# Performance work log

Measured on AMD Instinct MI355X. Metric: run time of the kernel, lower is better.

Reference implementation:

```python
import jax, jax.numpy as jnp
import numpy as np

N = 50000      # nodes
E = 800000     # edges
D = 96         # nfeat
C = 40         # nclass
NITE = 8       # train_nite / eval_nite
SMOOTH = 0.5   # smooth_fac


def setup_inputs() -> dict:
    key = jax.random.key(0)
    ks = jax.random.split(key, 6)
    x = jax.random.normal(ks[0], (N, D), dtype=jnp.float32)
    edge_row = jax.random.randint(ks[1], (E,), 0, N)
    edge_col = jax.random.randint(ks[2], (E,), 0, N)
    # ~1/avg_degree scale mimics a symmetrically normalized adjacency
    edge_vals = jax.random.uniform(ks[3], (E,), dtype=jnp.float32) / 16.0
    W_gc = jax.random.normal(ks[4], (D, D), dtype=jnp.float32) / jnp.sqrt(jnp.float32(D))
    b_gc = jnp.zeros((D,), dtype=jnp.float32)
    W_lin = jax.random.normal(ks[5], (D, C), dtype=jnp.float32) / jnp.sqrt(jnp.float32(D))
    return {"x": x, "edge_row": edge_row, "edge_col": edge_col,
            "edge_vals": edge_vals, "W_gc": W_gc, "b_gc": b_gc, "W_lin": W_lin}


def reference(x, edge_row, edge_col, edge_vals, W_gc, b_gc, W_lin):
    # One iteration: GraphConvolution (support = h @ W; out = A @ support + b),
    # smoothing skip connection, ReLU. Dropout is identity (eval / rate 0).
    def one_iter(h, _):
        support = h @ W_gc                                   # [N, D]
        msg = support[edge_col] * edge_vals[:, None]         # [E, D] gather + scale
        agg = jax.ops.segment_sum(msg, edge_row, num_segments=N) + b_gc  # [N, D]
        h_new = jax.nn.relu(SMOOTH * h + (1.0 - SMOOTH) * agg)
        return h_new, None

    h, _ = jax.lax.scan(one_iter, x, None, length=NITE)
    logits = h @ W_lin                                       # [N, C]
    return jax.nn.log_softmax(logits, axis=1)
```

## Files before the change

kernel.cpp:

```cpp
#include <hip/hip_runtime.h>

#define N_NODES 50000
#define E_EDGES 800000
#define D_FEAT  96
#define C_CLS   40
#define N_ITER  8

#define NCHUNK 49
#define NB     256
#define EPB    3125

typedef short bf16x8 __attribute__((ext_vector_type(8)));
typedef float f32x4  __attribute__((ext_vector_type(4)));
typedef float f32x2  __attribute__((ext_vector_type(2)));

#if defined(__has_builtin)
#if __has_builtin(__builtin_amdgcn_cvt_pk_f32_fp8) && __has_builtin(__builtin_amdgcn_cvt_pk_fp8_f32)
#define HAVE_FP8_CVT 1
#endif
#endif
#ifndef HAVE_FP8_CVT
#define HAVE_FP8_CVT 0
#endif

static __device__ __forceinline__ unsigned short f2bf(float f) {
    unsigned u = __float_as_uint(f);
    u = (u + 0x7FFF + ((u >> 16) & 1)) >> 16;
    return (unsigned short)u;
}

static __device__ __forceinline__ unsigned f32_to_fp8_manual(float f) {
    unsigned u = __float_as_uint(f);
    unsigned s = u >> 31;
    int e8 = (int)((u >> 23) & 0xFF) - 127 + 7;
    unsigned m23 = u & 0x7FFFFF;
    if (e8 <= 0) return s << 7;
    if (e8 >= 15) return (s << 7) | 0x7E;
    unsigned m = m23 >> 20;
    unsigned rem = m23 & 0xFFFFF;
    if (rem > 0x80000u || (rem == 0x80000u && (m & 1))) {
        m++;
        if (m == 8) { m = 0; e8++; if (e8 >= 15) return (s << 7) | 0x7E; }
    }
    return (s << 7) | ((unsigned)e8 << 3) | m;
}
static __device__ __forceinline__ float fp8_to_f32_manual(unsigned b) {
    unsigned s = (b >> 7) & 1, e = (b >> 3) & 0xF, m = b & 7;
    if (e == 0) return 0.0f;
    return __uint_as_float((s << 31) | ((e + 120) << 23) | (m << 20));
}
static __device__ __forceinline__ void fp8x4_dec(unsigned w, float* o) {
#if HAVE_FP8_CVT
    f32x2 lo = __builtin_amdgcn_cvt_pk_f32_fp8(w, false);
    f32x2 hi = __builtin_amdgcn_cvt_pk_f32_fp8(w, true);
    o[0] = lo[0]; o[1] = lo[1]; o[2] = hi[0]; o[3] = hi[1];
#else
    o[0] = fp8_to_f32_manual(w & 0xFF);
    o[1] = fp8_to_f32_manual((w >> 8) & 0xFF);
    o[2] = fp8_to_f32_manual((w >> 16) & 0xFF);
    o[3] = fp8_to_f32_manual((w >> 24) & 0xFF);
#endif
}
static __device__ __forceinline__ unsigned fp8x4_enc(float a, float b, float c, float d) {
#if HAVE_FP8_CVT
    unsigned w = __builtin_amdgcn_cvt_pk_fp8_f32(a, b, 0, false);
    w = __builtin_amdgcn_cvt_pk_fp8_f32(c, d, (int)w, true);
    return w;
#else
    return f32_to_fp8_manual(a) | (f32_to_fp8_manual(b) << 8) |
           (f32_to_fp8_manual(c) << 16) | (f32_to_fp8_manual(d) << 24);
#endif
}

__global__ __launch_bounds__(256) void k_count(const int* __restrict__ erow,
                                               int* __restrict__ cm) {
    __shared__ int lcnt[NCHUNK];
    int b = blockIdx.x, tid = threadIdx.x;
    if (tid < NCHUNK) lcnt[tid] = 0;
    __syncthreads();
    int base = b * EPB;
    for (int i = tid; i < EPB; i += 256)
        atomicAdd(&lcnt[erow[base + i] >> 10], 1);
    __syncthreads();
    if (tid < NCHUNK) cm[tid * NB + b] = lcnt[tid];
}

__global__ __launch_bounds__(1024) void k_cscan(int* __restrict__ cm) {
    __shared__ int sb[1024];
    const int TOT = NCHUNK * NB;
    const int PER = 13;
    int tid = threadIdx.x;
    int base = tid * PER;
    int v[PER];
    int s = 0;
    #pragma unroll
    for (int j = 0; j < PER; ++j) {
        int idx = base + j;
        v[j] = (idx < TOT) ? cm[idx] : 0;
        s += v[j];
    }
    sb[tid] = s;
    __syncthreads();
    for (int d = 1; d < 1024; d <<= 1) {
        int t = (tid >= d) ? sb[tid - d] : 0;
        __syncthreads();
        sb[tid] += t;
        __syncthreads();
    }
    int ex = sb[tid] - s;
    #pragma unroll
    for (int j = 0; j < PER; ++j) {
        int idx = base + j;
        if (idx < TOT) { cm[idx] = ex; ex += v[j]; }
    }
}

__global__ __launch_bounds__(256) void k_scatter_runs(const int* __restrict__ erow,
                                                      const int* __restrict__ ecol,
                                                      const float* __restrict__ ev,
                                                      const int* __restrict__ cm,
                                                      int2* __restrict__ stag) {
    __shared__ int lcur[NCHUNK];
    int b = blockIdx.x, tid = threadIdx.x;
    if (tid < NCHUNK) lcur[tid] = cm[tid * NB + b];
    __syncthreads();
    int base = b * EPB;
    for (int i = tid; i < EPB; i += 256) {
        int e = base + i;
        int r = erow[e];
        int c = r >> 10;
        int pos = atomicAdd(&lcur[c], 1);
        int2 s;
        s.x = (int)((unsigned)(ecol[e] & 0xFFFF) | ((unsigned)f2bf(ev[e]) << 16));
        s.y = r & 1023;
        stag[pos] = s;
    }
}

__global__ __launch_bounds__(1024) void k_chunk_csr(const int2* __restrict__ stag,
                                                    const int* __restrict__ cm,
                                                    unsigned* __restrict__ epk,
                                                    int* __restrict__ off) {
    __shared__ int lh[1024];
    __shared__ int lex[1024];
    __shared__ int sb[1024];
    int c = blockIdx.x, tid = threadIdx.x;
    int cb = cm[c * NB];
    int ce = (c + 1 < NCHUNK) ? cm[(c + 1) * NB] : E_EDGES;
    int m = ce - cb;

    lh[tid] = 0;
    __syncthreads();
    for (int i = tid; i < m; i += 1024) {
        int2 s = stag[cb + i];
        atomicAdd(&lh[s.y], 1);
    }
    __syncthreads();
    int v = lh[tid];
    sb[tid] = v;
    __syncthreads();
    for (int d = 1; d < 1024; d <<= 1) {
        int t = (tid >= d) ? sb[tid - d] : 0;
        __syncthreads();
        sb[tid] += t;
        __syncthreads();
    }
    int ex = sb[tid] - v;
    lex[tid] = ex;
    int node = c * 1024 + tid;
    if (node < N_NODES) off[node] = cb + ex;
    if (c == NCHUNK - 1 && tid == 0) off[N_NODES] = E_EDGES;
    __syncthreads();
    for (int i = tid; i < m; i += 1024) {
        int2 s = stag[cb + i];
        int pos = atomicAdd(&lex[s.y], 1);
        epk[cb + pos] = (unsigned)s.x;
    }
}

__global__ __launch_bounds__(256) void k_prep_w(const float* __restrict__ W,
                                                unsigned short* __restrict__ WB) {
    for (int idx = threadIdx.x; idx < 18 * 64; idx += 256) {
        int grp = idx >> 6;
        int lane = idx & 63;
        int t = grp / 3, s = grp - t * 3;
        int n = t * 16 + (lane & 15);
        int k0 = s * 32 + (lane >> 4) * 8;
        unsigned short* dst = WB + (size_t)idx * 8;
        #pragma unroll
        for (int j = 0; j < 8; ++j)
            dst[j] = f2bf(W[(k0 + j) * D_FEAT + n]);
    }
}

__global__ __launch_bounds__(256) void k_cvt_bf16(const float* __restrict__ src,
                                                  unsigned short* __restrict__ dst,
                                                  int n8) {
    int g = blockIdx.x * 256 + threadIdx.x;
    if (g >= n8) return;
    const float4* s4 = (const float4*)src + (size_t)g * 2;
    float4 x0 = s4[0], x1 = s4[1];
    float vals[8] = {x0.x, x0.y, x0.z, x0.w, x1.x, x1.y, x1.z, x1.w};
    uint4 pk; unsigned* pku = (unsigned*)&pk;
    #pragma unroll
    for (int w2 = 0; w2 < 4; ++w2) {
        unsigned lo = f2bf(vals[w2 * 2 + 0]);
        unsigned hi = f2bf(vals[w2 * 2 + 1]);
        pku[w2] = lo | (hi << 16);
    }
    *(uint4*)(dst + (size_t)g * 8) = pk;
}

__global__ __launch_bounds__(256) void k_matmul_mfma(
        const unsigned short* __restrict__ hb,
        const unsigned short* __restrict__ WB,
        unsigned char* __restrict__ support) {
    __shared__ float sm[64 * 100];
    int tid = threadIdx.x;
    int wave = tid >> 6, lane = tid & 63;
    int q = lane >> 4, c = lane & 15;
    int m0 = blockIdx.x * 64 + wave * 16;

    if (m0 < N_NODES) {
        const unsigned short* arow = hb + (size_t)(m0 + c) * D_FEAT + q * 8;
        bf16x8 a0 = *(const bf16x8*)(arow);
        bf16x8 a1 = *(const bf16x8*)(arow + 32);
        bf16x8 a2 = *(const bf16x8*)(arow + 64);
        #pragma unroll
        for (int t = 0; t < 6; ++t) {
            const unsigned short* bp = WB + ((size_t)(t * 3) * 64 + lane) * 8;
            bf16x8 b0 = *(const bf16x8*)(bp);
            bf16x8 b1 = *(const bf16x8*)(bp + 64 * 8);
            bf16x8 b2 = *(const bf16x8*)(bp + 128 * 8);
            f32x4 acc = {0.f, 0.f, 0.f, 0.f};
            acc = __builtin_amdgcn_mfma_f32_16x16x32_bf16(a0, b0, acc, 0, 0, 0);
            acc = __builtin_amdgcn_mfma_f32_16x16x32_bf16(a1, b1, acc, 0, 0, 0);
            acc = __builtin_amdgcn_mfma_f32_16x16x32_bf16(a2, b2, acc, 0, 0, 0);
            #pragma unroll
            for (int r = 0; r < 4; ++r)
                sm[(wave * 16 + q * 4 + r) * 100 + t * 16 + c] = acc[r];
        }
    }
    __syncthreads();

    #pragma unroll
    for (int oo = 0; oo < 3; ++oo) {
        int o = tid + oo * 256;
        int row = o / 12;
        int cb = (o - row * 12) * 8;
        int grow = blockIdx.x * 64 + row;
        if (grow < N_NODES) {
            const float* sp = sm + row * 100 + cb;
            uint2 pk;
            pk.x = fp8x4_enc(sp[0], sp[1], sp[2], sp[3]);
            pk.y = fp8x4_enc(sp[4], sp[5], sp[6], sp[7]);
            *(uint2*)(support + (size_t)grow * D_FEAT + cb) = pk;
        }
    }
}

__global__ __launch_bounds__(192) void k_agg(const int* __restrict__ off,
                                             const unsigned* __restrict__ epk,
                                             const unsigned char* __restrict__ support,
                                             const unsigned short* hin,
                                             const float* __restrict__ b,
                                             unsigned short* hout) {
    int gid = blockIdx.x * 192 + threadIdx.x;
    int n = gid / 6;
    int q = gid % 6;
    if (n >= N_NODES) return;

    int s = off[n];
    int e = off[n + 1];

    float acc[16];
    #pragma unroll
    for (int j = 0; j < 16; ++j) acc[j] = 0.0f;

    int i = s;
    for (; i < e && (i & 3); ++i) {
        unsigned p = epk[i];
        float v = __uint_as_float(p & 0xFFFF0000u);
        uint4 r = *(const uint4*)(support + (size_t)(p & 0xFFFFu) * D_FEAT + q * 16);
        float f[16];
        fp8x4_dec(r.x, f); fp8x4_dec(r.y, f + 4);
        fp8x4_dec(r.z, f + 8); fp8x4_dec(r.w, f + 12);
        #pragma unroll
        for (int j = 0; j < 16; ++j) acc[j] = fmaf(f[j], v, acc[j]);
    }
    for (; i + 4 <= e; i += 4) {
        uint4 pq = *(const uint4*)(epk + i);
        const unsigned* pp = (const unsigned*)&pq;
        uint4 r0 = *(const uint4*)(support + (size_t)(pp[0] & 0xFFFFu) * D_FEAT + q * 16);
        uint4 r1 = *(const uint4*)(support + (size_t)(pp[1] & 0xFFFFu) * D_FEAT + q * 16);
        uint4 r2 = *(const uint4*)(support + (size_t)(pp[2] & 0xFFFFu) * D_FEAT + q * 16);
        uint4 r3 = *(const uint4*)(support + (size_t)(pp[3] & 0xFFFFu) * D_FEAT + q * 16);
        float v0 = __uint_as_float(pp[0] & 0xFFFF0000u);
        float v1 = __uint_as_float(pp[1] & 0xFFFF0000u);
        float v2 = __uint_as_float(pp[2] & 0xFFFF0000u);
        float v3 = __uint_as_float(pp[3] & 0xFFFF0000u);
        float f[16];
        fp8x4_dec(r0.x, f); fp8x4_dec(r0.y, f + 4);
        fp8x4_dec(r0.z, f + 8); fp8x4_dec(r0.w, f + 12);
        #pragma unroll
        for (int j = 0; j < 16; ++j) acc[j] = fmaf(f[j], v0, acc[j]);
        fp8x4_dec(r1.x, f); fp8x4_dec(r1.y, f + 4);
        fp8x4_dec(r1.z, f + 8); fp8x4_dec(r1.w, f + 12);
        #pragma unroll
        for (int j = 0; j < 16; ++j) acc[j] = fmaf(f[j], v1, acc[j]);
        fp8x4_dec(r2.x, f); fp8x4_dec(r2.y, f + 4);
        fp8x4_dec(r2.z, f + 8); fp8x4_dec(r2.w, f + 12);
        #pragma unroll
        for (int j = 0; j < 16; ++j) acc[j] = fmaf(f[j], v2, acc[j]);
        fp8x4_dec(r3.x, f); fp8x4_dec(r3.y, f + 4);
        fp8x4_dec(r3.z, f + 8); fp8x4_dec(r3.w, f + 12);
        #pragma unroll
        for (int j = 0; j < 16; ++j) acc[j] = fmaf(f[j], v3, acc[j]);
    }
    for (; i < e; ++i) {
        unsigned p = epk[i];
        float v = __uint_as_float(p & 0xFFFF0000u);
        uint4 r = *(const uint4*)(support + (size_t)(p & 0xFFFFu) * D_FEAT + q * 16);
        float f[16];
        fp8x4_dec(r.x, f); fp8x4_dec(r.y, f + 4);
        fp8x4_dec(r.z, f + 8); fp8x4_dec(r.w, f + 12);
        #pragma unroll
        for (int j = 0; j < 16; ++j) acc[j] = fmaf(f[j], v, acc[j]);
    }

    const unsigned short* hrow = hin + (size_t)n * D_FEAT + q * 16;
    uint4 hq0 = *(const uint4*)(hrow);
    uint4 hq1 = *(const uint4*)(hrow + 8);
    const unsigned* hu0 = (const unsigned*)&hq0;
    const unsigned* hu1 = (const unsigned*)&hq1;
    const float* brow = b + q * 16;
    float og[16];
    #pragma unroll
    for (int w2 = 0; w2 < 4; ++w2) {
        float h0 = __uint_as_float(hu0[w2] << 16);
        float h1 = __uint_as_float(hu0[w2] & 0xFFFF0000u);
        og[w2*2+0] = fmaxf(0.5f * h0 + 0.5f * (acc[w2*2+0] + brow[w2*2+0]), 0.0f);
        og[w2*2+1] = fmaxf(0.5f * h1 + 0.5f * (acc[w2*2+1] + brow[w2*2+1]), 0.0f);
        float h2 = __uint_as_float(hu1[w2] << 16);
        float h3 = __uint_as_float(hu1[w2] & 0xFFFF0000u);
        og[8+w2*2+0] = fmaxf(0.5f * h2 + 0.5f * (acc[8+w2*2+0] + brow[8+w2*2+0]), 0.0f);
        og[8+w2*2+1] = fmaxf(0.5f * h3 + 0.5f * (acc[8+w2*2+1] + brow[8+w2*2+1]), 0.0f);
    }
    uint4 pk0, pk1;
    unsigned* pu0 = (unsigned*)&pk0;
    unsigned* pu1 = (unsigned*)&pk1;
    #pragma unroll
    for (int w2 = 0; w2 < 4; ++w2) {
        pu0[w2] = (unsigned)f2bf(og[w2*2+0]) | ((unsigned)f2bf(og[w2*2+1]) << 16);
        pu1[w2] = (unsigned)f2bf(og[8+w2*2+0]) | ((unsigned)f2bf(og[8+w2*2+1]) << 16);
    }
    unsigned short* orow = hout + (size_t)n * D_FEAT + q * 16;
    *(uint4*)(orow) = pk0;
    *(uint4*)(orow + 8) = pk1;
}

__global__ __launch_bounds__(256) void k_final(const unsigned short* __restrict__ hb,
                                               const float* __restrict__ Wg,
                                               float* __restrict__ out) {
    __shared__ float Wl[D_FEAT * C_CLS];
    {
        const float4* src = (const float4*)Wg;
        float4* dst = (float4*)Wl;
        for (int i = threadIdx.x; i < 960; i += 256) dst[i] = src[i];
    }
    __syncthreads();

    int n = blockIdx.x * 256 + threadIdx.x;
    if (n >= N_NODES) return;

    float acc[C_CLS];
    #pragma unroll
    for (int c = 0; c < C_CLS; ++c) acc[c] = 0.0f;

    const unsigned short* hrow = hb + (size_t)n * D_FEAT;
    for (int g = 0; g < 12; ++g) {
        uint4 hq = *(const uint4*)(hrow + g * 8);
        const unsigned* hu = (const unsigned*)&hq;
        float hv[8];
        #pragma unroll
        for (int w2 = 0; w2 < 4; ++w2) {
            hv[w2*2+0] = __uint_as_float(hu[w2] << 16);
            hv[w2*2+1] = __uint_as_float(hu[w2] & 0xFFFF0000u);
        }
        #pragma unroll
        for (int kk = 0; kk < 8; ++kk) {
            float hs = hv[kk];
            const float* wr = &Wl[(g * 8 + kk) * C_CLS];
            #pragma unroll
            for (int c4 = 0; c4 < 10; ++c4) {
                float4 w = *(const float4*)(wr + c4 * 4);
                acc[c4 * 4 + 0] = fmaf(hs, w.x, acc[c4 * 4 + 0]);
                acc[c4 * 4 + 1] = fmaf(hs, w.y, acc[c4 * 4 + 1]);
                acc[c4 * 4 + 2] = fmaf(hs, w.z, acc[c4 * 4 + 2]);
                acc[c4 * 4 + 3] = fmaf(hs, w.w, acc[c4 * 4 + 3]);
            }
        }
    }

    float m = acc[0];
    #pragma unroll
    for (int c = 1; c < C_CLS; ++c) m = fmaxf(m, acc[c]);
    float s = 0.0f;
    #pragma unroll
    for (int c = 0; c < C_CLS; ++c) s += expf(acc[c] - m);
    float lse = m + logf(s);

    float* orow = out + (size_t)n * C_CLS;
    #pragma unroll
    for (int c4 = 0; c4 < 10; ++c4)
        *(float4*)(orow + c4 * 4) =
            make_float4(acc[c4 * 4 + 0] - lse, acc[c4 * 4 + 1] - lse,
                        acc[c4 * 4 + 2] - lse, acc[c4 * 4 + 3] - lse);
}

static inline size_t align256(size_t x) { return (x + 255) & ~(size_t)255; }

extern "C" void kernel_launch(void* const* d_in, const int* in_sizes, int n_in,
                              void* d_out, int out_size, void* d_ws, size_t ws_size,
                              hipStream_t stream) {
    const float* x    = (const float*)d_in[0];
    const int*   erow = (const int*)  d_in[1];
    const int*   ecol = (const int*)  d_in[2];
    const float* ev   = (const float*)d_in[3];
    const float* Wgc  = (const float*)d_in[4];
    const float* bgc  = (const float*)d_in[5];
    const float* Wlin = (const float*)d_in[6];
    float* out = (float*)d_out;

    const size_t NF = (size_t)N_NODES * D_FEAT;
    char* ws = (char*)d_ws;
    unsigned short* hb         = (unsigned short*)ws; ws += align256(NF * 2);
    unsigned short* xb         = (unsigned short*)ws; ws += align256(NF * 2);
    unsigned char*  support_f8 = (unsigned char*)ws;  ws += align256(NF);
    unsigned*       epk        = (unsigned*)ws;       ws += align256((size_t)E_EDGES * 4);
    int2*           stag       = (int2*)ws;           ws += align256((size_t)E_EDGES * 8);
    unsigned short* WB         = (unsigned short*)ws; ws += align256((size_t)18 * 64 * 8 * 2);
    int*            off        = (int*)ws;            ws += align256((size_t)(N_NODES + 1) * 4);
    int*            cm         = (int*)ws;            ws += align256((size_t)NCHUNK * NB * 4);

    k_prep_w      <<<1, 256, 0, stream>>>(Wgc, WB);
    k_cvt_bf16    <<<(int)((NF / 8 + 255) / 256), 256, 0, stream>>>(x, xb, (int)(NF / 8));
    k_count       <<<NB, 256, 0, stream>>>(erow, cm);
    k_cscan       <<<1, 1024, 0, stream>>>(cm);
    k_scatter_runs<<<NB, 256, 0, stream>>>(erow, ecol, ev, cm, stag);
    k_chunk_csr   <<<NCHUNK, 1024, 0, stream>>>(stag, cm, epk, off);

    const int g_mm = (N_NODES + 63) / 64;
    const int g_ag = (N_NODES * 6 + 191) / 192;
    for (int it = 0; it < N_ITER; ++it) {
        const unsigned short* hin = (it == 0) ? xb : hb;
        k_matmul_mfma<<<g_mm, 256, 0, stream>>>(hin, WB, support_f8);
        k_agg        <<<g_ag, 192, 0, stream>>>(off, epk, support_f8, hin, bgc, hb);
    }
    k_final<<<(N_NODES + 255) / 256, 256, 0, stream>>>(hb, Wlin, out);
}
```

Before: 374.8 us.

## Split fp8 support into two column planes and aggregate each half separately

The matmul now writes the fp8 support matrix as two planes, each holding 48 feature columns per node in a 64-byte row. Aggregation runs as two kernel launches, one per plane, and each thread accumulates 8 features instead of 16. The smaller per-pass gather working set is meant to fit better in the per-XCD L2 cache, and the gather loop is software-pipelined to prefetch the next group of four neighbour rows. In exchange, the CSR edge list is read twice per iteration, there is an extra launch, and the padded rows add some memory footprint.

```diff
diff --git a/kernel.cpp b/kernel.cpp
--- a/kernel.cpp
+++ b/kernel.cpp
@@ -9,6 +9,8 @@
 #define NCHUNK 49
 #define NB     256
 #define EPB    3125
+
+#define PLANE  ((size_t)N_NODES * 64)
 
 typedef short bf16x8 __attribute__((ext_vector_type(8)));
 typedef float f32x4  __attribute__((ext_vector_type(4)));
@@ -72,6 +74,14 @@
 #endif
 }
 
+static __device__ __forceinline__ void fma8(uint2 r, float v, float* acc) {
+    float f[8];
+    fp8x4_dec(r.x, f);
+    fp8x4_dec(r.y, f + 4);
+    #pragma unroll
+    for (int j = 0; j < 8; ++j) acc[j] = fmaf(f[j], v, acc[j]);
+}
+
 __global__ __launch_bounds__(256) void k_count(const int* __restrict__ erow,
                                                int* __restrict__ cm) {
     __shared__ int lcnt[NCHUNK];
@@ -214,7 +224,7 @@
 __global__ __launch_bounds__(256) void k_matmul_mfma(
         const unsigned short* __restrict__ hb,
         const unsigned short* __restrict__ WB,
-        unsigned char* __restrict__ support) {
+        unsigned char* __restrict__ supp) {
     __shared__ float sm[64 * 100];
     int tid = threadIdx.x;
     int wave = tid >> 6, lane = tid & 63;
@@ -243,28 +253,31 @@
     }
     __syncthreads();
 
-    #pragma unroll
-    for (int oo = 0; oo < 3; ++oo) {
-        int o = tid + oo * 256;
-        int row = o / 12;
-        int cb = (o - row * 12) * 8;
+    for (int o = tid; o < 384; o += 256) {
+        int row = o / 6;
+        int rem = o - row * 6;
+        int plane = rem / 3;
+        int q3 = rem - plane * 3;
         int grow = blockIdx.x * 64 + row;
         if (grow < N_NODES) {
-            const float* sp = sm + row * 100 + cb;
-            uint2 pk;
-            pk.x = fp8x4_enc(sp[0], sp[1], sp[2], sp[3]);
-            pk.y = fp8x4_enc(sp[4], sp[5], sp[6], sp[7]);
-            *(uint2*)(support + (size_t)grow * D_FEAT + cb) = pk;
+            const float* sp = sm + row * 100 + plane * 48 + q3 * 16;
+            uint4 pk;
+            pk.x = fp8x4_enc(sp[0],  sp[1],  sp[2],  sp[3]);
+            pk.y = fp8x4_enc(sp[4],  sp[5],  sp[6],  sp[7]);
+            pk.z = fp8x4_enc(sp[8],  sp[9],  sp[10], sp[11]);
+            pk.w = fp8x4_enc(sp[12], sp[13], sp[14], sp[15]);
+            *(uint4*)(supp + (size_t)plane * PLANE + (size_t)grow * 64 + q3 * 16) = pk;
         }
     }
 }
 
-__global__ __launch_bounds__(192) void k_agg(const int* __restrict__ off,
-                                             const unsigned* __restrict__ epk,
-                                             const unsigned char* __restrict__ support,
-                                             const unsigned short* hin,
-                                             const float* __restrict__ b,
-                                             unsigned short* hout) {
+__global__ __launch_bounds__(192) void k_agg_half(const int* __restrict__ off,
+                                                  const unsigned* __restrict__ epk,
+                                                  const unsigned char* __restrict__ plane,
+                                                  const unsigned short* hin,
+                                                  const float* __restrict__ b,
+                                                  unsigned short* hout,
+                                                  int pc) {
     int gid = blockIdx.x * 192 + threadIdx.x;
     int n = gid / 6;
     int q = gid % 6;
@@ -273,90 +286,72 @@
     int s = off[n];
     int e = off[n + 1];
 
-    float acc[16];
-    #pragma unroll
-    for (int j = 0; j < 16; ++j) acc[j] = 0.0f;
+    float acc[8];
+    #pragma unroll
+    for (int j = 0; j < 8; ++j) acc[j] = 0.0f;
+
+    const int qb = q * 8;
 
     int i = s;
     for (; i < e && (i & 3); ++i) {
         unsigned p = epk[i];
         float v = __uint_as_float(p & 0xFFFF0000u);
-        uint4 r = *(const uint4*)(support + (size_t)(p & 0xFFFFu) * D_FEAT + q * 16);
-        float f[16];
-        fp8x4_dec(r.x, f); fp8x4_dec(r.y, f + 4);
-        fp8x4_dec(r.z, f + 8); fp8x4_dec(r.w, f + 12);
-        #pragma unroll
-        for (int j = 0; j < 16; ++j) acc[j] = fmaf(f[j], v, acc[j]);
-    }
-    for (; i + 4 <= e; i += 4) {
+        uint2 r = *(const uint2*)(plane + (size_t)(p & 0xFFFFu) * 64 + qb);
+        fma8(r, v, acc);
+    }
+    int ng = (e - i) >> 2;
+    if (ng > 0) {
         uint4 pq = *(const uint4*)(epk + i);
-        const unsigned* pp = (const unsigned*)&pq;
-        uint4 r0 = *(const uint4*)(support + (size_t)(pp[0] & 0xFFFFu) * D_FEAT + q * 16);
-        uint4 r1 = *(const uint4*)(support + (size_t)(pp[1] & 0xFFFFu) * D_FEAT + q * 16);
-        uint4 r2 = *(const uint4*)(support + (size_t)(pp[2] & 0xFFFFu) * D_FEAT + q * 16);
-        uint4 r3 = *(const uint4*)(support + (size_t)(pp[3] & 0xFFFFu) * D_FEAT + q * 16);
-        float v0 = __uint_as_float(pp[0] & 0xFFFF0000u);
-        float v1 = __uint_as_float(pp[1] & 0xFFFF0000u);
-        float v2 = __uint_as_float(pp[2] & 0xFFFF0000u);
-        float v3 = __uint_as_float(pp[3] & 0xFFFF0000u);
-        float f[16];
-        fp8x4_dec(r0.x, f); fp8x4_dec(r0.y, f + 4);
-        fp8x4_dec(r0.z, f + 8); fp8x4_dec(r0.w, f + 12);
-        #pragma unroll
-        for (int j = 0; j < 16; ++j) acc[j] = fmaf(f[j], v0, acc[j]);
-        fp8x4_dec(r1.x, f); fp8x4_dec(r1.y, f + 4);
-        fp8x4_dec(r1.z, f + 8); fp8x4_dec(r1.w, f + 12);
-        #pragma unroll
-        for (int j = 0; j < 16; ++j) acc[j] = fmaf(f[j], v1, acc[j]);
-        fp8x4_dec(r2.x, f); fp8x4_dec(r2.y, f + 4);
-        fp8x4_dec(r2.z, f + 8); fp8x4_dec(r2.w, f + 12);
-        #pragma unroll
-        for (int j = 0; j < 16; ++j) acc[j] = fmaf(f[j], v2, acc[j]);
-        fp8x4_dec(r3.x, f); fp8x4_dec(r3.y, f + 4);
-        fp8x4_dec(r3.z, f + 8); fp8x4_dec(r3.w, f + 12);
-        #pragma unroll
-        for (int j = 0; j < 16; ++j) acc[j] = fmaf(f[j], v3, acc[j]);
+        uint2 c0 = *(const uint2*)(plane + (size_t)(pq.x & 0xFFFFu) * 64 + qb);
+        uint2 c1 = *(const uint2*)(plane + (size_t)(pq.y & 0xFFFFu) * 64 + qb);
+        uint2 c2 = *(const uint2*)(plane + (size_t)(pq.z & 0xFFFFu) * 64 + qb);
+        uint2 c3 = *(const uint2*)(plane + (size_t)(pq.w & 0xFFFFu) * 64 + qb);
+        float v0 = __uint_as_float(pq.x & 0xFFFF0000u);
+        float v1 = __uint_as_float(pq.y & 0xFFFF0000u);
+        float v2 = __uint_as_float(pq.z & 0xFFFF0000u);
+        float v3 = __uint_as_float(pq.w & 0xFFFF0000u);
+        for (int g = 1; g < ng; ++g) {
+            uint4 pq2 = *(const uint4*)(epk + i + 4 * g);
+            uint2 n0 = *(const uint2*)(plane + (size_t)(pq2.x & 0xFFFFu) * 64 + qb);
+            uint2 n1 = *(const uint2*)(plane + (size_t)(pq2.y & 0xFFFFu) * 64 + qb);
+            uint2 n2 = *(const uint2*)(plane + (size_t)(pq2.z & 0xFFFFu) * 64 + qb);
+            uint2 n3 = *(const uint2*)(plane + (size_t)(pq2.w & 0xFFFFu) * 64 + qb);
+            fma8(c0, v0, acc); fma8(c1, v1, acc);
+            fma8(c2, v2, acc); fma8(c3, v3, acc);
+            c0 = n0; c1 = n1; c2 = n2; c3 = n3;
+            v0 = __uint_as_float(pq2.x & 0xFFFF0000u);
+            v1 = __uint_as_float(pq2.y & 0xFFFF0000u);
+            v2 = __uint_as_float(pq2.z & 0xFFFF0000u);
+            v3 = __uint_as_float(pq2.w & 0xFFFF0000u);
+        }
+        fma8(c0, v0, acc); fma8(c1, v1, acc);
+        fma8(c2, v2, acc); fma8(c3, v3, acc);
+        i += 4 * ng;
     }
     for (; i < e; ++i) {
         unsigned p = epk[i];
         float v = __uint_as_float(p & 0xFFFF0000u);
-        uint4 r = *(const uint4*)(support + (size_t)(p & 0xFFFFu) * D_FEAT + q * 16);
-        float f[16];
-        fp8x4_dec(r.x, f); fp8x4_dec(r.y, f + 4);
-        fp8x4_dec(r.z, f + 8); fp8x4_dec(r.w, f + 12);
-        #pragma unroll
-        for (int j = 0; j < 16; ++j) acc[j] = fmaf(f[j], v, acc[j]);
-    }
-
-    const unsigned short* hrow = hin + (size_t)n * D_FEAT + q * 16;
-    uint4 hq0 = *(const uint4*)(hrow);
-    uint4 hq1 = *(const uint4*)(hrow + 8);
-    const unsigned* hu0 = (const unsigned*)&hq0;
-    const unsigned* hu1 = (const unsigned*)&hq1;
-    const float* brow = b + q * 16;
-    float og[16];
+        uint2 r = *(const uint2*)(plane + (size_t)(p & 0xFFFFu) * 64 + qb);
+        fma8(r, v, acc);
+    }
+
+    int col = pc + qb;
+    uint4 hq = *(const uint4*)(hin + (size_t)n * D_FEAT + col);
+    const unsigned* hu = (const unsigned*)&hq;
+    const float* brow = b + col;
+    float og[8];
     #pragma unroll
     for (int w2 = 0; w2 < 4; ++w2) {
-        float h0 = __uint_as_float(hu0[w2] << 16);
-        float h1 = __uint_as_float(hu0[w2] & 0xFFFF0000u);
+        float h0 = __uint_as_float(hu[w2] << 16);
+        float h1 = __uint_as_float(hu[w2] & 0xFFFF0000u);
         og[w2*2+0] = fmaxf(0.5f * h0 + 0.5f * (acc[w2*2+0] + brow[w2*2+0]), 0.0f);
         og[w2*2+1] = fmaxf(0.5f * h1 + 0.5f * (acc[w2*2+1] + brow[w2*2+1]), 0.0f);
-        float h2 = __uint_as_float(hu1[w2] << 16);
-        float h3 = __uint_as_float(hu1[w2] & 0xFFFF0000u);
-        og[8+w2*2+0] = fmaxf(0.5f * h2 + 0.5f * (acc[8+w2*2+0] + brow[8+w2*2+0]), 0.0f);
-        og[8+w2*2+1] = fmaxf(0.5f * h3 + 0.5f * (acc[8+w2*2+1] + brow[8+w2*2+1]), 0.0f);
-    }
-    uint4 pk0, pk1;
-    unsigned* pu0 = (unsigned*)&pk0;
-    unsigned* pu1 = (unsigned*)&pk1;
-    #pragma unroll
-    for (int w2 = 0; w2 < 4; ++w2) {
-        pu0[w2] = (unsigned)f2bf(og[w2*2+0]) | ((unsigned)f2bf(og[w2*2+1]) << 16);
-        pu1[w2] = (unsigned)f2bf(og[8+w2*2+0]) | ((unsigned)f2bf(og[8+w2*2+1]) << 16);
-    }
-    unsigned short* orow = hout + (size_t)n * D_FEAT + q * 16;
-    *(uint4*)(orow) = pk0;
-    *(uint4*)(orow + 8) = pk1;
+    }
+    uint4 pk; unsigned* pku = (unsigned*)&pk;
+    #pragma unroll
+    for (int w2 = 0; w2 < 4; ++w2)
+        pku[w2] = (unsigned)f2bf(og[w2*2+0]) | ((unsigned)f2bf(og[w2*2+1]) << 16);
+    *(uint4*)(hout + (size_t)n * D_FEAT + col) = pk;
 }
 
 __global__ __launch_bounds__(256) void k_final(const unsigned short* __restrict__ hb,
@@ -436,7 +431,7 @@
     char* ws = (char*)d_ws;
     unsigned short* hb         = (unsigned short*)ws; ws += align256(NF * 2);
     unsigned short* xb         = (unsigned short*)ws; ws += align256(NF * 2);
-    unsigned char*  support_f8 = (unsigned char*)ws;  ws += align256(NF);
+    unsigned char*  supp       = (unsigned char*)ws;  ws += align256(2 * PLANE);
     unsigned*       epk        = (unsigned*)ws;       ws += align256((size_t)E_EDGES * 4);
     int2*           stag       = (int2*)ws;           ws += align256((size_t)E_EDGES * 8);
     unsigned short* WB         = (unsigned short*)ws; ws += align256((size_t)18 * 64 * 8 * 2);
@@ -454,8 +449,9 @@
     const int g_ag = (N_NODES * 6 + 191) / 192;
     for (int it = 0; it < N_ITER; ++it) {
         const unsigned short* hin = (it == 0) ? xb : hb;
-        k_matmul_mfma<<<g_mm, 256, 0, stream>>>(hin, WB, support_f8);
-        k_agg        <<<g_ag, 192, 0, stream>>>(off, epk, support_f8, hin, bgc, hb);
+        k_matmul_mfma<<<g_mm, 256, 0, stream>>>(hin, WB, supp);
+        k_agg_half   <<<g_ag, 192, 0, stream>>>(off, epk, supp,         hin, bgc, hb, 0);
+        k_agg_half   <<<g_ag, 192, 0, stream>>>(off, epk, supp + PLANE, hin, bgc, hb, 48);
     }
     k_final<<<(N_NODES + 255) / 256, 256, 0, stream>>>(hb, Wlin, out);
 }
```

Measured after the change: 438.5 us. 17.0% more time.
